# Kernel optimization log

Hardware: AMD Instinct MI355X
Metric: run time of the kernel (lower is better)

Reference implementation:

```python
import jax, jax.numpy as jnp
import numpy as np

M, DEPTH, L, B = 4, 8, 256, 8192
TOTAL_NODES = 2 ** DEPTH - 1  # balanced binary tree: sum 2^d, d<DEPTH
BETA, GAMMA, LAMBD, EC_CE_W = 1.0, 1.0, 1.0, 1.0
TEMP = 0.07


def setup_inputs() -> dict:
    key = jax.random.key(0)
    k1, k2 = jax.random.split(key)
    xs = jax.random.normal(k1, (M, B, L), dtype=jnp.float32)
    tree_emb = jax.random.normal(k2, (M, TOTAL_NODES, 2 * L), dtype=jnp.float32)
    return {"xs": xs, "tree_emb": tree_emb}


def _align_loss(query, keybook, dist):
    # argmin over codebook axis, one-hot @ keybook == gather
    idx = jnp.argmin(dist, axis=1)
    quantised = keybook[idx]
    e_latent = jnp.mean((jax.lax.stop_gradient(quantised) - query) ** 2)
    q_latent = jnp.mean((quantised - jax.lax.stop_gradient(query)) ** 2)
    loss = e_latent + q_latent
    q_st = query + jax.lax.stop_gradient(quantised - query)  # straight-through
    return idx, q_st, loss


def _vq_level(x, e, parent_idx):
    # squared euclidean distance (B, K)
    dist = (x ** 2).sum(1, keepdims=True) + (e ** 2).sum(1)[None, :] - 2.0 * (x @ e.T)
    if parent_idx is not None:
        Bn, K = dist.shape
        mask = jnp.full((Bn, K), jnp.inf, dtype=dist.dtype)
        cols = jnp.stack([parent_idx * 2, parent_idx * 2 + 1], axis=1)  # (B, 2)
        rows = jnp.arange(Bn)[:, None]
        mask = mask.at[rows, cols].set(0.0)
        dist_t = dist + mask
    else:
        dist_t = dist
    idx, z, loss_ec = _align_loss(x, e, dist_t)
    _, _, loss_ce = _align_loss(e, x, dist_t.T)
    return idx, z, loss_ec + EC_CE_W * loss_ce


def _tree_wasserstein(p1, p2):
    p1 = p1 / (p1.sum() + 1e-8)
    p2 = p2 / (p2.sum() + 1e-8)
    d = jnp.float32(0.0)
    while p1.shape[0] > 1:  # static shape loop (halving)
        d = d + jnp.abs(p1 - p2).sum()
        p1 = p1.reshape(-1, 2).sum(1)
        p2 = p2.reshape(-1, 2).sum(1)
    return d


def _info_nce(za, zb):
    na = za / jnp.maximum(jnp.linalg.norm(za, axis=-1, keepdims=True), 1e-12)
    nb = zb / jnp.maximum(jnp.linalg.norm(zb, axis=-1, keepdims=True), 1e-12)
    logits = (na @ nb.T) / TEMP  # (B, B)
    return -jnp.mean(jnp.diagonal(jax.nn.log_softmax(logits, axis=-1)))


def _forward(xs, tree_emb):
    mu_all = tree_emb[..., :L]       # (M, TOTAL_NODES, L)
    logvar_all = tree_emb[..., L:]
    kl = 0.5 * jnp.sum(jnp.exp(logvar_all) + mu_all ** 2 - 1.0 - logvar_all)
    kl_loss = kl / (M * TOTAL_NODES * L)

    all_idx = [[None] * DEPTH for _ in range(M)]
    all_z = [[None] * DEPTH for _ in range(M)]
    vq_total = jnp.float32(0.0)
    for m in range(M):
        for d in range(DEPTH):
            off, K = 2 ** d - 1, 2 ** d
            e = mu_all[m, off:off + K]           # (K, L)
            parent = all_idx[m][d - 1] if d > 0 else None
            idx, z, vq_loss = _vq_level(xs[m], e, parent)
            all_idx[m][d], all_z[m][d] = idx, z
            vq_total = vq_total + vq_loss

    align = jnp.float32(0.0)
    for d in range(DEPTH):  # all levels are ot_levels by default
        K = 2 ** d
        for m in range(M - 1):
            n = m + 1
            pi_m = jnp.zeros((K,), jnp.float32).at[all_idx[m][d]].add(1.0)
            pi_n = jnp.zeros((K,), jnp.float32).at[all_idx[n][d]].add(1.0)
            align = align + GAMMA * _tree_wasserstein(pi_m, pi_n)
            align = align + LAMBD * _info_nce(all_z[m][d], all_z[n][d])

    total = vq_total + BETA * kl_loss + align
    idx_all = jnp.stack([jnp.stack(r) for r in all_idx])  # (M, DEPTH, B) int
    z_all = jnp.stack([jnp.stack(r) for r in all_z])      # (M, DEPTH, B, L)
    return idx_all, z_all, total


def reference(xs, tree_emb):
    return _forward(xs, tree_emb)
```

## Files before the change

kernel.cpp:

```cpp
#include <hip/hip_runtime.h>

#define NM     4
#define NDEPTH 8
#define NL     256
#define NB     8192
#define NNODES 255
#define STAB_PP 21845
#define ZBASE  (NM*NDEPTH*NB)
#define TOTAL_IDX (ZBASE + (size_t)NM*NDEPTH*NB*NL)
#define INFPACK (0x7F800000ULL << 32)
#define NROWS (NM*NDEPTH*NB)
#define CACHED_NODES 31
#define NODE_W 292

typedef float f32x4 __attribute__((ext_vector_type(4)));

__device__ __constant__ int c_pref[8] = {0,1,5,21,85,341,1365,5461};

__device__ __forceinline__ double wred(double v) {
  v += __shfl_xor(v, 1, 64);
  v += __shfl_xor(v, 2, 64);
  v += __shfl_xor(v, 4, 64);
  v += __shfl_xor(v, 8, 64);
  v += __shfl_xor(v, 16, 64);
  v += __shfl_xor(v, 32, 64);
  return v;
}
__device__ __forceinline__ void wred2(double& a, double& b) {
  #pragma unroll
  for (int m = 1; m <= 32; m <<= 1) {
    double ta = __shfl_xor(a, m, 64);
    double tb = __shfl_xor(b, m, 64);
    a += ta; b += tb;
  }
}
__device__ __forceinline__ void wred2_16(double& a, double& b) {
  #pragma unroll
  for (int m = 1; m <= 8; m <<= 1) {
    double ta = __shfl_xor(a, m, 16);
    double tb = __shfl_xor(b, m, 16);
    a += ta; b += tb;
  }
}
__device__ __forceinline__ double dot4d(const float4 a, const float4 b) {
  return (double)a.x*(double)b.x + (double)a.y*(double)b.y
       + (double)a.z*(double)b.z + (double)a.w*(double)b.w;
}
__device__ __forceinline__ double dot16dx(const double* xd,
    const f32x4 a, const f32x4 b, const f32x4 c, const f32x4 d) {
  double s0 = xd[0]*(double)a.x + xd[1]*(double)a.y;
  double s1 = xd[2]*(double)a.z + xd[3]*(double)a.w;
  double s2 = xd[4]*(double)b.x + xd[5]*(double)b.y;
  double s3 = xd[6]*(double)b.z + xd[7]*(double)b.w;
  double s4 = xd[8]*(double)c.x + xd[9]*(double)c.y;
  double s5 = xd[10]*(double)c.z + xd[11]*(double)c.w;
  double s6 = xd[12]*(double)d.x + xd[13]*(double)d.y;
  double s7 = xd[14]*(double)d.z + xd[15]*(double)d.w;
  return ((s0 + s1) + (s2 + s3)) + ((s4 + s5) + (s6 + s7));
}
__device__ __forceinline__ unsigned long long packf(float dist, int b) {
  return ((unsigned long long)__float_as_uint(dist) << 32) | (unsigned int)b;
}

static constexpr size_t OFF_EN   = 0;
static constexpr size_t OFF_KLP  = OFF_EN   + 1020*8;
static constexpr size_t OFF_PD   = OFF_KLP  + 1020*8;
static constexpr size_t OFF_STAB = OFF_PD   + (size_t)262144*8;
static constexpr size_t OFF_REC  = OFF_STAB + (size_t)65535*8;
static constexpr size_t OFF_RCE  = OFF_REC  + 32*8;
static constexpr size_t OFF_RNC  = OFF_RCE  + 32*8;
static constexpr size_t OFF_RW   = OFF_RNC  + 24*8;
static constexpr size_t OFF_CNT  = OFF_RW   + 24*8;
static constexpr size_t OFF_IDX  = OFF_CNT  + 1020*4;
static constexpr size_t OFF_NC   = OFF_IDX  + (size_t)262144*4;


__global__ __launch_bounds__(256) void k_prep(const float* __restrict__ tree,
    double* __restrict__ en, double* __restrict__ klp, float* __restrict__ nc) {
  int w = (int)((blockIdx.x*blockDim.x + threadIdx.x) >> 6);
  int lane = threadIdx.x & 63;
  if (w >= NM*NNODES) return;
  const float* row = tree + (size_t)w*(2*NL);
  float4 mu = ((const float4*)row)[lane];
  float4 lv = ((const float4*)(row + NL))[lane];
  double s2 = dot4d(mu, mu);
  double kp = exp((double)lv.x)+exp((double)lv.y)+exp((double)lv.z)+exp((double)lv.w)
            - (double)lv.x-(double)lv.y-(double)lv.z-(double)lv.w + s2 - 4.0;
  double s2t = s2, kpt = kp;
  wred2(s2t, kpt);
  double inv = 1.0 / fmax(sqrt(s2t), 1e-12);
  float4 o;
  o.x=(float)(mu.x*inv); o.y=(float)(mu.y*inv); o.z=(float)(mu.z*inv); o.w=(float)(mu.w*inv);
  ((float4*)(nc + (size_t)w*NL))[lane] = o;
  if (lane == 0) { en[w] = s2t; klp[w] = kpt; }
}

__global__ __launch_bounds__(256) void k_decide(
    const float* __restrict__ xs, const float* __restrict__ tree,
    const double* __restrict__ en, float* __restrict__ out,
    int* __restrict__ idxws, float2* __restrict__ pd)
{
  __shared__ float s_tree[CACHED_NODES * NODE_W];
  __shared__ double s_en[NNODES];
  int t = threadIdx.x;
  int blk = blockIdx.x;
  int m = (int)(((unsigned)blk * 16) >> 13);
  const float* treem = tree + (size_t)m*NNODES*(2*NL);
  for (int j = t; j < CACHED_NODES*64; j += 256) {
    int node = j >> 6, w4 = j & 63;
    *(f32x4*)&s_tree[node*NODE_W + w4*4] =
        *(const f32x4*)(treem + (size_t)node*(2*NL) + w4*4);
  }
  if (t < NNODES) s_en[t] = en[m*NNODES + t];
  __syncthreads();

  int wv = t >> 6, lane = t & 63;
  int g = lane >> 4, l = lane & 15;
  int row = blk*16 + wv*4 + g;
  int b = row & (NB-1);
  int lw = l*4;

  const float* xrow = xs + (size_t)row*NL;
  f32x4 x0 = __builtin_nontemporal_load((const f32x4*)(xrow + lw));
  f32x4 x1 = __builtin_nontemporal_load((const f32x4*)(xrow + lw + 64));
  f32x4 x2 = __builtin_nontemporal_load((const f32x4*)(xrow + lw + 128));
  f32x4 x3 = __builtin_nontemporal_load((const f32x4*)(xrow + lw + 192));
  double xd[16];
  xd[0]=(double)x0.x; xd[1]=(double)x0.y; xd[2]=(double)x0.z; xd[3]=(double)x0.w;
  xd[4]=(double)x1.x; xd[5]=(double)x1.y; xd[6]=(double)x1.z; xd[7]=(double)x1.w;
  xd[8]=(double)x2.x; xd[9]=(double)x2.y; xd[10]=(double)x2.z; xd[11]=(double)x2.w;
  xd[12]=(double)x3.x; xd[13]=(double)x3.y; xd[14]=(double)x3.z; xd[15]=(double)x3.w;

  f32x4 e0 = *(const f32x4*)&s_tree[lw];
  f32x4 e1 = *(const f32x4*)&s_tree[lw + 64];
  f32x4 e2 = *(const f32x4*)&s_tree[lw + 128];
  f32x4 e3 = *(const f32x4*)&s_tree[lw + 192];
  double xn;
  {
    double n0 = xd[0]*xd[0] + xd[1]*xd[1];
    double n1 = xd[2]*xd[2] + xd[3]*xd[3];
    double n2 = xd[4]*xd[4] + xd[5]*xd[5];
    double n3 = xd[6]*xd[6] + xd[7]*xd[7];
    double n4 = xd[8]*xd[8] + xd[9]*xd[9];
    double n5 = xd[10]*xd[10] + xd[11]*xd[11];
    double n6 = xd[12]*xd[12] + xd[13]*xd[13];
    double n7 = xd[14]*xd[14] + xd[15]*xd[15];
    xn = ((n0 + n1) + (n2 + n3)) + ((n4 + n5) + (n6 + n7));
  }
  double rr = dot16dx(xd, e0, e1, e2, e3);
  wred2_16(xn, rr);
  double dd0 = xn + s_en[0] - 2.0*rr;
  int oi = (m*NDEPTH)*NB + b;
  if (l == 0) { idxws[oi] = 0; pd[oi] = make_float2((float)dd0,(float)dd0); }

  f32x4 c0a = *(const f32x4*)&s_tree[1*NODE_W + lw];
  f32x4 c0b = *(const f32x4*)&s_tree[1*NODE_W + lw + 64];
  f32x4 c0c = *(const f32x4*)&s_tree[1*NODE_W + lw + 128];
  f32x4 c0d = *(const f32x4*)&s_tree[1*NODE_W + lw + 192];
  f32x4 c1a = *(const f32x4*)&s_tree[2*NODE_W + lw];
  f32x4 c1b = *(const f32x4*)&s_tree[2*NODE_W + lw + 64];
  f32x4 c1c = *(const f32x4*)&s_tree[2*NODE_W + lw + 128];
  f32x4 c1d = *(const f32x4*)&s_tree[2*NODE_W + lw + 192];

  {
    float* zo = out + (size_t)ZBASE + (size_t)oi*NL;
    *(f32x4*)(zo + lw)       = e0;
    *(f32x4*)(zo + lw + 64)  = e1;
    *(f32x4*)(zo + lw + 128) = e2;
    *(f32x4*)(zo + lw + 192) = e3;
  }

  int pk = 0;
  #pragma unroll
  for (int d = 1; d < NDEPTH; ++d) {
    int n0 = (1 << d) - 1 + 2*pk;
    double r0 = dot16dx(xd, c0a, c0b, c0c, c0d);
    double r1 = dot16dx(xd, c1a, c1b, c1c, c1d);
    wred2_16(r0, r1);
    double en0 = s_en[n0], en1 = s_en[n0+1];
    double d0 = xn + en0 - 2.0*r0;
    double d1 = xn + en1 - 2.0*r1;
    bool p1s = (d1 < d0);
    int kc = 2*pk + (p1s ? 1 : 0);
    f32x4 zs0 = p1s ? c1a : c0a;
    f32x4 zs1 = p1s ? c1b : c0b;
    f32x4 zs2 = p1s ? c1c : c0c;
    f32x4 zs3 = p1s ? c1d : c0d;
    oi = (m*NDEPTH + d)*NB + b;
    pk = kc;
    if (d < NDEPTH-1) {
      int nn = (1 << (d+1)) - 1 + 2*pk;
      if (d + 1 <= 4) {
        c0a = *(const f32x4*)&s_tree[nn*NODE_W + lw];
        c0b = *(const f32x4*)&s_tree[nn*NODE_W + lw + 64];
        c0c = *(const f32x4*)&s_tree[nn*NODE_W + lw + 128];
        c0d = *(const f32x4*)&s_tree[nn*NODE_W + lw + 192];
        c1a = *(const f32x4*)&s_tree[(nn+1)*NODE_W + lw];
        c1b = *(const f32x4*)&s_tree[(nn+1)*NODE_W + lw + 64];
        c1c = *(const f32x4*)&s_tree[(nn+1)*NODE_W + lw + 128];
        c1d = *(const f32x4*)&s_tree[(nn+1)*NODE_W + lw + 192];
      } else {
        const float* n0p = treem + (size_t)nn*(2*NL);
        const float* n1p = n0p + 2*NL;
        c0a = *(const f32x4*)(n0p + lw);
        c0b = *(const f32x4*)(n0p + lw + 64);
        c0c = *(const f32x4*)(n0p + lw + 128);
        c0d = *(const f32x4*)(n0p + lw + 192);
        c1a = *(const f32x4*)(n1p + lw);
        c1b = *(const f32x4*)(n1p + lw + 64);
        c1c = *(const f32x4*)(n1p + lw + 128);
        c1d = *(const f32x4*)(n1p + lw + 192);
      }
    }
    {
      float* zo = out + (size_t)ZBASE + (size_t)oi*NL;
      *(f32x4*)(zo + lw)       = zs0;
      *(f32x4*)(zo + lw + 64)  = zs1;
      *(f32x4*)(zo + lw + 128) = zs2;
      *(f32x4*)(zo + lw + 192) = zs3;
    }
    if (l == 0) { idxws[oi] = kc; pd[oi] = make_float2((float)d0,(float)d1); }
  }
}

__global__ __launch_bounds__(256) void k_mid(
    const float* __restrict__ xs, const float* __restrict__ tree,
    const float2* __restrict__ pd, const int* __restrict__ idxws,
    const float* __restrict__ nc,
    unsigned int* __restrict__ cnt, double* __restrict__ rec,
    double* __restrict__ rce, double* __restrict__ stab,
    float* __restrict__ out)
{
  __shared__ unsigned long long nmin[128*8];
  __shared__ unsigned int hc[128*8];
  __shared__ double sh[256];
  int t = threadIdx.x;
  if (blockIdx.x < 32) {
    int bid = blockIdx.x; int m = bid >> 3, d = bid & 7;
    int K = 1 << d, off = K - 1;
    for (int i = t; i < K*8; i += 256) { nmin[i] = INFPACK; hc[i] = 0u; }
    __syncthreads();
    int st = t & 7;
    double a = 0;
    if (d == 0) {
      const float2* pp = pd + (size_t)(m*NDEPTH)*NB;
      float* ob = out + (size_t)(m*NDEPTH)*NB;
      for (int b = t; b < NB; b += 256) {
        float2 v = pp[b]; a += (double)v.x;
        atomicMin(&nmin[st], packf(v.x, b));
        ob[b] = 0.0f;
      }
    } else {
      const int* pidx = idxws + (m*NDEPTH + d - 1)*NB;
      const int* cidx = idxws + (m*NDEPTH + d)*NB;
      const float2* pp = pd + (size_t)(m*NDEPTH + d)*NB;
      float* ob = out + (size_t)(m*NDEPTH + d)*NB;
      for (int b = t; b < NB; b += 256) {
        int pk = pidx[b]; float2 v = pp[b];
        int cc = cidx[b];
        a += (double)fminf(v.x, v.y);
        atomicMin(&nmin[(2*pk  )*8 + st], packf(v.x, b));
        atomicMin(&nmin[(2*pk+1)*8 + st], packf(v.y, b));
        atomicAdd(&hc[cc*8 + st], 1u);
        ob[b] = (float)cc;
      }
    }
    sh[t] = a; __syncthreads();
    for (int s = 128; s > 0; s >>= 1) { if (t < s) sh[t] += sh[t+s]; __syncthreads(); }
    if (t == 0) rec[bid] = sh[0];
    for (int i = t; i < K; i += 256) {
      unsigned long long mn = nmin[i*8];
      unsigned int c = hc[i*8];
      #pragma unroll
      for (int s = 1; s < 8; ++s) { mn = min(mn, nmin[i*8+s]); c += hc[i*8+s]; }
      nmin[i*8] = mn;
      cnt[m*NNODES + off + i] = (d == 0) ? (unsigned)NB : c;
    }
    __syncthreads();
    int wv = t >> 6, ln = t & 63;
    for (int i = wv; i < K; i += 4) {
      unsigned int b2 = (unsigned int)(nmin[i*8] & 0xFFFFFFFFULL);
      const float4* xr = (const float4*)(xs + ((size_t)m*NB + b2)*NL);
      const float4* er = (const float4*)(tree + (size_t)(m*NNODES + off + i)*(2*NL));
      float4 xv = xr[ln], ev = er[ln];
      double dx=(double)xv.x-(double)ev.x, dy=(double)xv.y-(double)ev.y;
      double dz=(double)xv.z-(double)ev.z, dw=(double)xv.w-(double)ev.w;
      double s = wred(dx*dx + dy*dy + dz*dz + dw*dw);
      if (ln == 0) sh[i] = s;
    }
    __syncthreads();
    double c2 = (t < K) ? sh[t] : 0.0;
    __syncthreads();
    sh[t] = c2; __syncthreads();
    for (int s = 128; s > 0; s >>= 1) { if (t < s) sh[t] += sh[t+s]; __syncthreads(); }
    if (t == 0) rce[bid] = sh[0];
  } else {
    int wid0 = (int)((blockIdx.x - 32)*4 + (t >> 6));
    int lane = t & 63;
    int nw = (int)(gridDim.x - 32)*4;
    for (int w = wid0; w < 3*STAB_PP; w += nw) {
      int p = w / STAB_PP, r = w - p*STAB_PP;
      int d = 0;
      while (d < 7 && r >= c_pref[d+1]) ++d;
      int q = r - c_pref[d]; int K = 1 << d; int off = K - 1;
      int i = q >> d, j = q & (K - 1);
      float4 av = ((const float4*)(nc + (size_t)(p*NNODES + off + i)*NL))[lane];
      float4 bv = ((const float4*)(nc + (size_t)((p+1)*NNODES + off + j)*NL))[lane];
      double s = wred(dot4d(av, bv));
      if (lane == 0) stab[w] = s / 0.07;
    }
  }
}

__global__ __launch_bounds__(256) void k_tail(const double* __restrict__ stab,
    const unsigned int* __restrict__ cnt, const int* __restrict__ idxws,
    double* __restrict__ rnc, double* __restrict__ rw) {
  int t = threadIdx.x;
  if (blockIdx.x < 24) {
    int bid = blockIdx.x; int d = bid / 3, p = bid % 3;
    int K = 1 << d, off = K - 1;
    __shared__ unsigned int cnl[128];
    __shared__ double lsel[128];
    __shared__ double sh[256];
    if (t < K) cnl[t] = cnt[(p+1)*NNODES + off + t];
    __syncthreads();
    const double* sb = stab + (size_t)p*STAB_PP + c_pref[d];
    if (t < K) {
      const double* srow = sb + (size_t)t*K;
      double mx = -1e300;
      for (int j = 0; j < K; ++j) if (cnl[j] > 0u) { double v = srow[j]; if (v > mx) mx = v; }
      double s = 0;
      for (int j = 0; j < K; ++j) if (cnl[j] > 0u) s += (double)cnl[j]*exp(srow[j] - mx);
      lsel[t] = mx + log(s);
    }
    __syncthreads();
    const int* im  = idxws + (p*NDEPTH + d)*NB;
    const int* in_ = idxws + ((p+1)*NDEPTH + d)*NB;
    double a = 0;
    for (int b = t; b < NB; b += 256) {
      int cm = im[b], cn2 = in_[b];
      a += sb[(size_t)cm*K + cn2] - lsel[cm];
    }
    sh[t] = a; __syncthreads();
    for (int s = 128; s > 0; s >>= 1) { if (t < s) sh[t] += sh[t+s]; __syncthreads(); }
    if (t == 0) rnc[bid] = sh[0];
  } else {
    int bid = blockIdx.x - 24; int d = bid / 3, p = bid % 3;
    int K = 1 << d, off = K - 1;
    __shared__ double A[128], Bv[128], Rd[128];
    __shared__ double Wsh;
    if (t < 128) {
      A[t]  = (t < K) ? (double)cnt[p*NNODES + off + t]     : 0.0;
      Bv[t] = (t < K) ? (double)cnt[(p+1)*NNODES + off + t] : 0.0;
    }
    if (t == 0) Wsh = 0.0;
    __syncthreads();
    if (t < 128) Rd[t] = A[t];
    __syncthreads();
    for (int s = 64; s > 0; s >>= 1) { if (t < s) Rd[t] += Rd[t+s]; __syncthreads(); }
    double s1 = Rd[0];
    __syncthreads();
    if (t < 128) Rd[t] = Bv[t];
    __syncthreads();
    for (int s = 64; s > 0; s >>= 1) { if (t < s) Rd[t] += Rd[t+s]; __syncthreads(); }
    double s2 = Rd[0];
    __syncthreads();
    double i1 = 1.0/(s1 + 1e-8), i2 = 1.0/(s2 + 1e-8);
    if (t < K) { A[t] *= i1; Bv[t] *= i2; }
    __syncthreads();
    for (int n = K; n > 1; n >>= 1) {
      if (t < 128) Rd[t] = (t < n) ? fabs(A[t] - Bv[t]) : 0.0;
      __syncthreads();
      for (int s = 64; s > 0; s >>= 1) { if (t < s) Rd[t] += Rd[t+s]; __syncthreads(); }
      if (t == 0) Wsh += Rd[0];
      int h = n >> 1;
      double na = 0, nb = 0;
      if (t < h) { na = A[2*t] + A[2*t+1]; nb = Bv[2*t] + Bv[2*t+1]; }
      __syncthreads();
      if (t < h) { A[t] = na; Bv[t] = nb; }
      __syncthreads();
    }
    if (t == 0) rw[bid] = Wsh;
  }
}

__global__ __launch_bounds__(256) void k_final(const double* __restrict__ klp,
    const double* __restrict__ rec, const double* __restrict__ rce,
    const double* __restrict__ rnc, const double* __restrict__ rw,
    float* __restrict__ out) {
  __shared__ double sh[256];
  int t = threadIdx.x;
  double a = 0;
  for (int i = t; i < NM*NNODES; i += 256) a += klp[i];
  sh[t] = a; __syncthreads();
  for (int s = 128; s > 0; s >>= 1) { if (t < s) sh[t] += sh[t+s]; __syncthreads(); }
  if (t == 0) {
    double kl = 0.5*sh[0] / ((double)NM*NNODES*NL);
    double vq = 0;
    for (int m = 0; m < NM; ++m)
      for (int d = 0; d < NDEPTH; ++d) {
        double K = (double)(1 << d);
        vq += 2.0*rec[m*NDEPTH + d]/((double)NB*NL)
            + 2.0*rce[m*NDEPTH + d]/(K*(double)NL);
      }
    double align = 0;
    for (int d = 0; d < NDEPTH; ++d)
      for (int p = 0; p < 3; ++p)
        align += rw[d*3 + p] - rnc[d*3 + p]/(double)NB;
    out[TOTAL_IDX] = (float)(vq + kl + align);
  }
}

extern "C" void kernel_launch(void* const* d_in, const int* in_sizes, int n_in,
                              void* d_out, int out_size, void* d_ws, size_t ws_size,
                              hipStream_t stream) {
  (void)in_sizes; (void)n_in; (void)out_size; (void)ws_size;
  const float* xs   = (const float*)d_in[0];
  const float* tree = (const float*)d_in[1];
  float* out = (float*)d_out;
  char* ws = (char*)d_ws;

  double* en   = (double*)(ws + OFF_EN);
  double* klp  = (double*)(ws + OFF_KLP);
  float2* pd   = (float2*)(ws + OFF_PD);
  double* stab = (double*)(ws + OFF_STAB);
  double* rec  = (double*)(ws + OFF_REC);
  double* rce  = (double*)(ws + OFF_RCE);
  double* rnc  = (double*)(ws + OFF_RNC);
  double* rw   = (double*)(ws + OFF_RW);
  unsigned int* cnt = (unsigned int*)(ws + OFF_CNT);
  int* idxws   = (int*)(ws + OFF_IDX);
  float* nc    = (float*)(ws + OFF_NC);

  k_prep   <<<255, 256, 0, stream>>>(tree, en, klp, nc);
  k_decide <<<2048, 256, 0, stream>>>(xs, tree, en, out, idxws, pd);
  k_mid    <<<2048, 256, 0, stream>>>(xs, tree, pd, idxws, nc, cnt, rec, rce, stab, out);
  k_tail   <<<48, 256, 0, stream>>>(stab, cnt, idxws, rnc, rw);
  k_final  <<<1, 256, 0, stream>>>(klp, rec, rce, rnc, rw, out);
}
```

Before: 165.6 us.

## Move quantised-z output writes from tree walk into mid kernel gather

Removes the 256-float z-vector stores from the tree-walk kernel, leaving it to produce only indices and distances. The z output (M*DEPTH*B rows of L floats) is instead written by a new block range in k_mid that gathers each selected codebook row by index and copies it out, running alongside the stab and per-level reduction blocks. This is meant to shorten the latency-bound walk and overlap the large write traffic with other work. The cost is an extra read of idxws plus a gather from the tree embeddings, and the stab loop now assumes a fixed count of 480 blocks.

Result: no change. 165.8 us (+0.1%).

```diff
diff --git a/kernel.cpp b/kernel.cpp
--- a/kernel.cpp
+++ b/kernel.cpp
@@ -95,9 +95,9 @@
   if (lane == 0) { en[w] = s2t; klp[w] = kpt; }
 }
 
-__global__ __launch_bounds__(256) void k_decide(
+__global__ __launch_bounds__(256) void k_walk(
     const float* __restrict__ xs, const float* __restrict__ tree,
-    const double* __restrict__ en, float* __restrict__ out,
+    const double* __restrict__ en,
     int* __restrict__ idxws, float2* __restrict__ pd)
 {
   __shared__ float s_tree[CACHED_NODES * NODE_W];
@@ -162,14 +162,6 @@
   f32x4 c1c = *(const f32x4*)&s_tree[2*NODE_W + lw + 128];
   f32x4 c1d = *(const f32x4*)&s_tree[2*NODE_W + lw + 192];
 
-  {
-    float* zo = out + (size_t)ZBASE + (size_t)oi*NL;
-    *(f32x4*)(zo + lw)       = e0;
-    *(f32x4*)(zo + lw + 64)  = e1;
-    *(f32x4*)(zo + lw + 128) = e2;
-    *(f32x4*)(zo + lw + 192) = e3;
-  }
-
   int pk = 0;
   #pragma unroll
   for (int d = 1; d < NDEPTH; ++d) {
@@ -182,10 +174,6 @@
     double d1 = xn + en1 - 2.0*r1;
     bool p1s = (d1 < d0);
     int kc = 2*pk + (p1s ? 1 : 0);
-    f32x4 zs0 = p1s ? c1a : c0a;
-    f32x4 zs1 = p1s ? c1b : c0b;
-    f32x4 zs2 = p1s ? c1c : c0c;
-    f32x4 zs3 = p1s ? c1d : c0d;
     oi = (m*NDEPTH + d)*NB + b;
     pk = kc;
     if (d < NDEPTH-1) {
@@ -212,13 +200,6 @@
         c1d = *(const f32x4*)(n1p + lw + 192);
       }
     }
-    {
-      float* zo = out + (size_t)ZBASE + (size_t)oi*NL;
-      *(f32x4*)(zo + lw)       = zs0;
-      *(f32x4*)(zo + lw + 64)  = zs1;
-      *(f32x4*)(zo + lw + 128) = zs2;
-      *(f32x4*)(zo + lw + 192) = zs3;
-    }
     if (l == 0) { idxws[oi] = kc; pd[oi] = make_float2((float)d0,(float)d1); }
   }
 }
@@ -294,10 +275,10 @@
     sh[t] = c2; __syncthreads();
     for (int s = 128; s > 0; s >>= 1) { if (t < s) sh[t] += sh[t+s]; __syncthreads(); }
     if (t == 0) rce[bid] = sh[0];
-  } else {
+  } else if (blockIdx.x < 512) {
     int wid0 = (int)((blockIdx.x - 32)*4 + (t >> 6));
     int lane = t & 63;
-    int nw = (int)(gridDim.x - 32)*4;
+    const int nw = 480*4;
     for (int w = wid0; w < 3*STAB_PP; w += nw) {
       int p = w / STAB_PP, r = w - p*STAB_PP;
       int d = 0;
@@ -308,6 +289,18 @@
       float4 bv = ((const float4*)(nc + (size_t)((p+1)*NNODES + off + j)*NL))[lane];
       double s = wred(dot4d(av, bv));
       if (lane == 0) stab[w] = s / 0.07;
+    }
+  } else {
+    int gw = (int)((blockIdx.x - 512)*4 + (t >> 6));
+    int lane = t & 63;
+    const int nw = 1536*4;
+    for (int row = gw; row < NROWS; row += nw) {
+      int m = row >> 16;
+      int d = (row >> 13) & 7;
+      int k = idxws[row];
+      int node = (1 << d) - 1 + k;
+      f32x4 v = ((const f32x4*)(tree + (size_t)(m*NNODES + node)*(2*NL)))[lane];
+      ((f32x4*)(out + (size_t)ZBASE + (size_t)row*NL))[lane] = v;
     }
   }
 }
@@ -432,9 +425,9 @@
   int* idxws   = (int*)(ws + OFF_IDX);
   float* nc    = (float*)(ws + OFF_NC);
 
-  k_prep   <<<255, 256, 0, stream>>>(tree, en, klp, nc);
-  k_decide <<<2048, 256, 0, stream>>>(xs, tree, en, out, idxws, pd);
-  k_mid    <<<2048, 256, 0, stream>>>(xs, tree, pd, idxws, nc, cnt, rec, rce, stab, out);
-  k_tail   <<<48, 256, 0, stream>>>(stab, cnt, idxws, rnc, rw);
-  k_final  <<<1, 256, 0, stream>>>(klp, rec, rce, rnc, rw, out);
-}
+  k_prep  <<<255, 256, 0, stream>>>(tree, en, klp, nc);
+  k_walk  <<<2048, 256, 0, stream>>>(xs, tree, en, idxws, pd);
+  k_mid   <<<2048, 256, 0, stream>>>(xs, tree, pd, idxws, nc, cnt, rec, rce, stab, out);
+  k_tail  <<<48, 256, 0, stream>>>(stab, cnt, idxws, rnc, rw);
+  k_final <<<1, 256, 0, stream>>>(klp, rec, rce, rnc, rw, out);
+}
```
